# Optimization experiments

Hardware: AMD Instinct MI355X
Metric: run time of the kernel (lower is better)

The kernel has to match this reference:

```python
import jax, jax.numpy as jnp
import numpy as np
from jax import lax

B, N, D = 8, 16384, 64
NPOINT, NSAMPLE, RADIUS = 1024, 32, 0.1
MLP = [3 + D, 64, 64, 128]
BN_EPS = 1e-5


def setup_inputs() -> dict:
    key = jax.random.key(0)
    ks = jax.random.split(key, 8)
    inp = {
        'xyz': jax.random.uniform(ks[0], (B, 3, N), dtype=jnp.float32),
        'points': jax.random.normal(ks[1], (B, D, N), dtype=jnp.float32),
    }
    for i, (cin, cout) in enumerate(zip(MLP[:-1], MLP[1:]), start=1):
        inp[f'w{i}'] = jax.random.normal(ks[1 + i], (cout, cin), dtype=jnp.float32) / np.sqrt(cin)
        inp[f'b{i}'] = jnp.zeros((cout,), jnp.float32)
        inp[f'g{i}'] = jnp.ones((cout,), jnp.float32)
        inp[f'be{i}'] = jnp.zeros((cout,), jnp.float32)
    return inp


def farthest_point_sample(xyz, npoint):
    # xyz: (B, N, 3). Deterministic start at index 0 (torch uses randint).
    b, n, _ = xyz.shape

    def step(carry, _):
        distance, farthest = carry  # (B,N), (B,)
        centroid = jnp.take_along_axis(xyz, farthest[:, None, None], axis=1)  # (B,1,3)
        dist = jnp.sum((xyz - centroid) ** 2, axis=-1)  # (B,N)
        distance = jnp.minimum(distance, dist)
        new_far = jnp.argmax(distance, axis=-1).astype(jnp.int32)
        return (distance, new_far), farthest

    init = (jnp.full((b, n), 1e10, xyz.dtype), jnp.zeros((b,), jnp.int32))
    _, idxs = lax.scan(step, init, None, length=npoint)  # (npoint, B)
    return idxs.T  # (B, npoint)


def query_ball_point(radius, nsample, xyz, new_xyz):
    # xyz: (B,N,3), new_xyz: (B,S,3) -> (B,S,nsample) int32
    b, n, _ = xyz.shape
    # squared pairwise distances (B,S,N)
    sqr = (jnp.sum(new_xyz ** 2, -1)[:, :, None]
           + jnp.sum(xyz ** 2, -1)[:, None, :]
           - 2.0 * jnp.einsum('bsc,bnc->bsn', new_xyz, xyz))
    group_idx = jnp.where(sqr > radius ** 2, n, jnp.arange(n, dtype=jnp.int32))
    group_idx = jnp.sort(group_idx, axis=-1)[:, :, :nsample]
    first = group_idx[:, :, :1]
    return jnp.where(group_idx == n, first, group_idx)


def reference(xyz, points, w1, b1, g1, be1, w2, b2, g2, be2, w3, b3, g3, be3):
    xyz_t = xyz.transpose(0, 2, 1)      # (B,N,3)
    pts_t = points.transpose(0, 2, 1)   # (B,N,D)
    bsz = xyz_t.shape[0]

    fps_idx = farthest_point_sample(xyz_t, NPOINT)          # (B,S)
    bidx2 = jnp.arange(bsz)[:, None]
    new_xyz = xyz_t[bidx2, fps_idx]                          # (B,S,3)

    idx = query_ball_point(RADIUS, NSAMPLE, xyz_t, new_xyz)  # (B,S,ns)
    bidx3 = jnp.arange(bsz)[:, None, None]
    grouped_xyz = xyz_t[bidx3, idx] - new_xyz[:, :, None, :]  # (B,S,ns,3)
    grouped_pts = pts_t[bidx3, idx]                           # (B,S,ns,D)
    feat = jnp.concatenate([grouped_xyz, grouped_pts], axis=-1)  # (B,S,ns,C)

    for w, b, g, be in ((w1, b1, g1, be1), (w2, b2, g2, be2), (w3, b3, g3, be3)):
        feat = jnp.einsum('bsnc,oc->bsno', feat, w) + b
        mean = feat.mean(axis=(0, 1, 2))
        var = feat.var(axis=(0, 1, 2))  # biased, as torch BN uses for normalization
        feat = (feat - mean) * lax.rsqrt(var + BN_EPS) * g + be
        feat = jax.nn.relu(feat)

    new_points = feat.max(axis=2)  # max over nsample -> (B,S,Cout)
    return new_xyz.transpose(0, 2, 1), new_points.transpose(0, 2, 1)
```

## Files before the change

kernel.cpp:

```cpp
#include <hip/hip_runtime.h>
#include <hip/hip_bf16.h>
#include <stdint.h>

#define BATCH 8
#define NPTS  16384
#define DIMF  64
#define SPTS  1024
#define NSAMP 32
#define MTOT  (BATCH*SPTS*NSAMP)

__device__ __forceinline__ float bfu_lo(uint32_t u){ return __uint_as_float(u<<16); }
__device__ __forceinline__ float bfu_hi(uint32_t u){ return __uint_as_float(u & 0xffff0000u); }
__device__ __forceinline__ uint16_t f2bf(float f){
  __hip_bfloat16 h = __float2bfloat16(f);
  uint16_t u; __builtin_memcpy(&u, &h, 2); return u;
}

__global__ __launch_bounds__(512, 2) void fps_kernel(const float* __restrict__ xyz,
                                                     float* __restrict__ out0,
                                                     const float* __restrict__ pts,
                                                     float* __restrict__ ptsT){
  if (blockIdx.x >= BATCH){
    __shared__ float tile[64][65];
    int bb = blockIdx.x - BATCH;
    int b  = bb >> 8;
    int n0 = (bb & 255) << 6;
    const float* src = pts + (size_t)b*DIMF*NPTS;
    float* dst = ptsT + (size_t)b*NPTS*DIMF;
    int t = threadIdx.x;
    int cn = t & 63, cw = t >> 6;
#pragma unroll
    for (int j=0;j<8;j++){
      int c = cw + j*8;
      tile[c][cn] = src[(size_t)c*NPTS + n0 + cn];
    }
    __syncthreads();
#pragma unroll
    for (int j=0;j<8;j++){
      int nl = cw + j*8;
      dst[(size_t)(n0+nl)*DIMF + cn] = tile[cn][nl];
    }
    return;
  }
  int b = blockIdx.x;
  const float* X = xyz + (size_t)b*3*NPTS;
  int t = threadIdx.x;
  int lane = t & 63, wid = t >> 6;
  float px[32], py[32], pz[32], dst[32];
#pragma unroll
  for (int k=0;k<32;k++){
    int n = t + (k<<9);
    px[k]=X[n]; py[k]=X[NPTS+n]; pz[k]=X[2*NPTS+n];
    dst[k]=1e10f;
  }
  __shared__ float rv[2][8];
  __shared__ int   ri[2][8];
  int far = 0;
  float* o = out0 + (size_t)b*3*SPTS;
  for (int s=0;s<SPTS;s++){
    float cx = X[far], cy = X[NPTS+far], cz = X[2*NPTS+far];
    if (t==0){ o[s]=cx; o[SPTS+s]=cy; o[2*SPTS+s]=cz; }
    if (s==SPTS-1) break;
    float best = -1.0f; int bi = 0x7fffffff;
#pragma unroll
    for (int k=0;k<32;k++){
      float dx=__fsub_rn(px[k],cx), dy=__fsub_rn(py[k],cy), dz=__fsub_rn(pz[k],cz);
      float d = __fadd_rn(__fadd_rn(__fmul_rn(dx,dx),__fmul_rn(dy,dy)),__fmul_rn(dz,dz));
      d = fminf(dst[k], d); dst[k] = d;
      if (d > best){ best = d; bi = t + (k<<9); }
    }
#pragma unroll
    for (int off=1; off<64; off<<=1){
      float ov = __shfl_xor(best, off);
      int   oi = __shfl_xor(bi, off);
      if (ov > best || (ov == best && oi < bi)){ best = ov; bi = oi; }
    }
    int p = s & 1;
    if (lane==0){ rv[p][wid]=best; ri[p][wid]=bi; }
    __syncthreads();
    float v = rv[p][lane&7]; int j = ri[p][lane&7];
#pragma unroll
    for (int off=1; off<8; off<<=1){
      float ov = __shfl_xor(v, off);
      int   oj = __shfl_xor(j, off);
      if (ov > v || (ov == v && oj < j)){ v = ov; j = oj; }
    }
    far = j;
  }
}

__global__ __launch_bounds__(256) void ball_kernel(const float* __restrict__ xyz,
                                                   const float* __restrict__ newxyz,
                                                   int* __restrict__ idxo){
  int b  = blockIdx.x >> 5;
  int sc = blockIdx.x & 31;
  const float* X  = xyz + (size_t)b*3*NPTS;
  int t = threadIdx.x, lane = t & 63, w = t >> 6;
  __shared__ float lx[512], ly[512], lz[512], ls[512];
  __shared__ int done;
  if (t==0) done = 0;
  const float rsq = 0.01f;
  float nx[8], ny[8], nz[8], sn[8];
  int cnt[8], first[8];
  int sbase = sc*32 + w*8;
#pragma unroll
  for (int q=0;q<8;q++){
    int s = sbase + q;
    nx[q] = newxyz[(size_t)b*3*SPTS + s];
    ny[q] = newxyz[(size_t)b*3*SPTS + SPTS + s];
    nz[q] = newxyz[(size_t)b*3*SPTS + 2*SPTS + s];
    sn[q] = __fadd_rn(__fadd_rn(__fmul_rn(nx[q],nx[q]),__fmul_rn(ny[q],ny[q])),
                      __fmul_rn(nz[q],nz[q]));
    cnt[q]=0; first[q]=0;
  }
  __syncthreads();
  for (int T=0;T<32;T++){
    {
      float ax = X[T*512 + t], ay = X[NPTS + T*512 + t], az = X[2*NPTS + T*512 + t];
      lx[t]=ax; ly[t]=ay; lz[t]=az;
      ls[t] = __fadd_rn(__fadd_rn(__fmul_rn(ax,ax),__fmul_rn(ay,ay)),__fmul_rn(az,az));
      float bx = X[T*512 + t + 256], by = X[NPTS + T*512 + t + 256], bz = X[2*NPTS + T*512 + t + 256];
      lx[t+256]=bx; ly[t+256]=by; lz[t+256]=bz;
      ls[t+256] = __fadd_rn(__fadd_rn(__fmul_rn(bx,bx),__fmul_rn(by,by)),__fmul_rn(bz,bz));
    }
    __syncthreads();
#pragma unroll
    for (int q=0;q<8;q++){
      if (cnt[q] >= NSAMP) continue;
      int s = sbase + q;
      int* op = idxo + ((size_t)(b*SPTS + s))*NSAMP;
      for (int c=0;c<8;c++){
        int li = c*64 + lane;
        float dot = fmaf(nz[q], lz[li], fmaf(ny[q], ly[li], __fmul_rn(nx[q], lx[li])));
        float sq  = __fsub_rn(__fadd_rn(sn[q], ls[li]), __fmul_rn(2.0f, dot));
        bool in = (sq <= rsq);
        unsigned long long m = __ballot(in);
        if (cnt[q]==0 && m) first[q] = T*512 + c*64 + (int)__builtin_ctzll(m);
        if (in){
          int slot = cnt[q] + (int)__popcll(m & ((1ull<<lane)-1ull));
          if (slot < NSAMP) op[slot] = T*512 + li;
        }
        cnt[q] += (int)__popcll(m);
        if (cnt[q] >= NSAMP){ if (lane==0) atomicAdd(&done,1); break; }
      }
    }
    __syncthreads();
    if (done >= 32) break;
  }
#pragma unroll
  for (int q=0;q<8;q++){
    if (cnt[q] < NSAMP){
      int s = sbase + q;
      int* op = idxo + ((size_t)(b*SPTS + s))*NSAMP;
      if (lane >= cnt[q] && lane < NSAMP) op[lane] = first[q];
    }
  }
}

__global__ __launch_bounds__(256) void gemm1_kernel(const float* __restrict__ xyz,
                                                    const float* __restrict__ ptsT,
                                                    const int* __restrict__ idx,
                                                    const float* __restrict__ newxyz,
                                                    const float* __restrict__ w1,
                                                    const float* __restrict__ b1,
                                                    uint16_t* __restrict__ y1,
                                                    float* __restrict__ gsum,
                                                    float* __restrict__ gsq){
  __shared__ float As[128*69];
  __shared__ float Ws[67*64];
  __shared__ float bias[64];
  __shared__ int   ndx[128];
  __shared__ float nxs[4][3];
  int t = threadIdx.x;
  int g0 = blockIdx.x*128;
  if (t < 128) ndx[t] = idx[g0 + t];
  if (t < 12){
    int grp = t/3, c = t%3;
    int bs = (g0>>5) + grp; int b = bs>>10, s = bs & 1023;
    nxs[grp][c] = newxyz[(size_t)b*3*SPTS + c*SPTS + s];
  }
  if (t < 64) bias[t] = b1[t];
  for (int e=t; e<67*64; e+=256){ int k=e>>6, c=e&63; Ws[k*64+c] = w1[c*67+k]; }
  __syncthreads();
  {
    int r = t>>1, h = t&1;
    int n = ndx[r];
    int bs = (g0>>5) + (r>>5); int b = bs>>10;
    const float* pr = ptsT + ((size_t)(b*NPTS + n))*64 + h*32;
    float* ar = As + r*69;
    if (h==0){
      int grp = r>>5;
      ar[0] = __fsub_rn(xyz[(size_t)b*3*NPTS + n],          nxs[grp][0]);
      ar[1] = __fsub_rn(xyz[(size_t)b*3*NPTS + NPTS + n],   nxs[grp][1]);
      ar[2] = __fsub_rn(xyz[(size_t)b*3*NPTS + 2*NPTS + n], nxs[grp][2]);
    }
    float* ap = ar + 3 + h*32;
#pragma unroll
    for (int j=0;j<8;j++){
      float4 v = *(const float4*)(pr + j*4);
      ap[j*4+0]=v.x; ap[j*4+1]=v.y; ap[j*4+2]=v.z; ap[j*4+3]=v.w;
    }
  }
  __syncthreads();
  int rg = t>>3, cg = t&7;
  float acc[4][8];
#pragma unroll
  for (int i=0;i<4;i++)
#pragma unroll
    for (int j=0;j<8;j++) acc[i][j]=0.f;
  for (int k=0;k<67;k++){
    float a0 = As[(rg*4+0)*69+k];
    float a1 = As[(rg*4+1)*69+k];
    float a2 = As[(rg*4+2)*69+k];
    float a3 = As[(rg*4+3)*69+k];
    const float* wr = Ws + k*64 + cg*8;
    float4 w0 = *(const float4*)wr;
    float4 w1v = *(const float4*)(wr+4);
    float wj[8] = {w0.x,w0.y,w0.z,w0.w,w1v.x,w1v.y,w1v.z,w1v.w};
#pragma unroll
    for (int j=0;j<8;j++){
      acc[0][j] = fmaf(a0, wj[j], acc[0][j]);
      acc[1][j] = fmaf(a1, wj[j], acc[1][j]);
      acc[2][j] = fmaf(a2, wj[j], acc[2][j]);
      acc[3][j] = fmaf(a3, wj[j], acc[3][j]);
    }
  }
  float ps[8], pq[8];
#pragma unroll
  for (int j=0;j<8;j++){ ps[j]=0.f; pq[j]=0.f; }
#pragma unroll
  for (int i=0;i<4;i++){
    int gr = g0 + rg*4 + i;
    uint16_t* yr = y1 + (size_t)gr*64 + cg*8;
    uint4 vv; uint32_t u[4]; float vj[8];
#pragma unroll
    for (int j=0;j<8;j++){
      vj[j] = acc[i][j] + bias[cg*8+j];
      ps[j] += vj[j]; pq[j] += vj[j]*vj[j];
    }
#pragma unroll
    for (int j=0;j<4;j++)
      u[j] = (uint32_t)f2bf(vj[2*j]) | ((uint32_t)f2bf(vj[2*j+1])<<16);
    vv.x=u[0]; vv.y=u[1]; vv.z=u[2]; vv.w=u[3];
    *(uint4*)yr = vv;
  }
  __syncthreads();
  float* red = As;
#pragma unroll
  for (int j=0;j<8;j++){
    red[rg*65 + cg*8 + j]        = ps[j];
    red[2080 + rg*65 + cg*8 + j] = pq[j];
  }
  __syncthreads();
  if (t < 64){
    float s=0.f, q=0.f;
    for (int r=0;r<32;r++){ s += red[r*65+t]; q += red[2080 + r*65 + t]; }
    int kb = (blockIdx.x & 15) * 128;
    atomicAdd(&gsum[kb + t], s); atomicAdd(&gsq[kb + t], q);
  }
}

__global__ __launch_bounds__(256) void gemm2_kernel(const uint16_t* __restrict__ yin,
                                                    const float* __restrict__ w2,
                                                    const float* __restrict__ b2,
                                                    const float* __restrict__ gsumi,
                                                    const float* __restrict__ gsqi,
                                                    const float* __restrict__ gi,
                                                    const float* __restrict__ bei,
                                                    uint16_t* __restrict__ yout,
                                                    float* __restrict__ gsum,
                                                    float* __restrict__ gsq){
  __shared__ float As[128*65];
  __shared__ float Ws[64*64];
  __shared__ float bias[64], sc[64], sh[64];
  int t = threadIdx.x;
  int g0 = blockIdx.x*128;
  if (t < 64){
    bias[t]=b2[t];
    double ssum=0.0, ssq=0.0;
    for (int k2=0;k2<16;k2++){ ssum += (double)gsumi[k2*128+t]; ssq += (double)gsqi[k2*128+t]; }
    double mean = ssum / (double)MTOT;
    double var  = ssq / (double)MTOT - mean*mean;
    double sv   = (double)gi[t] / sqrt(var + 1e-5);
    sc[t] = (float)sv;
    sh[t] = (float)((double)bei[t] - mean*sv);
  }
  for (int e=t; e<64*64; e+=256){ int k=e>>6, c=e&63; Ws[k*64+c] = w2[c*64+k]; }
  __syncthreads();
  {
    int r = t>>1, h = t&1;
    const uint4* yv = (const uint4*)(yin + (size_t)(g0+r)*64 + h*32);
    float* ar = As + r*65 + h*32;
#pragma unroll
    for (int j=0;j<4;j++){
      uint4 u = yv[j];
      uint32_t vv[4] = {u.x,u.y,u.z,u.w};
#pragma unroll
      for (int m=0;m<4;m++){
        int c = h*32 + j*8 + m*2;
        ar[j*8+m*2]   = fmaxf(fmaf(bfu_lo(vv[m]), sc[c],   sh[c]),   0.f);
        ar[j*8+m*2+1] = fmaxf(fmaf(bfu_hi(vv[m]), sc[c+1], sh[c+1]), 0.f);
      }
    }
  }
  __syncthreads();
  int rg = t>>3, cg = t&7;
  float acc[4][8];
#pragma unroll
  for (int i=0;i<4;i++)
#pragma unroll
    for (int j=0;j<8;j++) acc[i][j]=0.f;
  for (int k=0;k<64;k++){
    float a0 = As[(rg*4+0)*65+k];
    float a1 = As[(rg*4+1)*65+k];
    float a2 = As[(rg*4+2)*65+k];
    float a3 = As[(rg*4+3)*65+k];
    const float* wr = Ws + k*64 + cg*8;
    float4 w0 = *(const float4*)wr;
    float4 w1v = *(const float4*)(wr+4);
    float wj[8] = {w0.x,w0.y,w0.z,w0.w,w1v.x,w1v.y,w1v.z,w1v.w};
#pragma unroll
    for (int j=0;j<8;j++){
      acc[0][j] = fmaf(a0, wj[j], acc[0][j]);
      acc[1][j] = fmaf(a1, wj[j], acc[1][j]);
      acc[2][j] = fmaf(a2, wj[j], acc[2][j]);
      acc[3][j] = fmaf(a3, wj[j], acc[3][j]);
    }
  }
  float ps[8], pq[8];
#pragma unroll
  for (int j=0;j<8;j++){ ps[j]=0.f; pq[j]=0.f; }
#pragma unroll
  for (int i=0;i<4;i++){
    int gr = g0 + rg*4 + i;
    uint16_t* yr = yout + (size_t)gr*64 + cg*8;
    uint4 vv; uint32_t u[4]; float vj[8];
#pragma unroll
    for (int j=0;j<8;j++){
      vj[j] = acc[i][j] + bias[cg*8+j];
      ps[j] += vj[j]; pq[j] += vj[j]*vj[j];
    }
#pragma unroll
    for (int j=0;j<4;j++)
      u[j] = (uint32_t)f2bf(vj[2*j]) | ((uint32_t)f2bf(vj[2*j+1])<<16);
    vv.x=u[0]; vv.y=u[1]; vv.z=u[2]; vv.w=u[3];
    *(uint4*)yr = vv;
  }
  __syncthreads();
  float* red = As;
#pragma unroll
  for (int j=0;j<8;j++){
    red[rg*65 + cg*8 + j]        = ps[j];
    red[2080 + rg*65 + cg*8 + j] = pq[j];
  }
  __syncthreads();
  if (t < 64){
    float s=0.f, q=0.f;
    for (int r=0;r<32;r++){ s += red[r*65+t]; q += red[2080 + r*65 + t]; }
    int kb = (blockIdx.x & 15) * 128;
    atomicAdd(&gsum[kb + t], s); atomicAdd(&gsq[kb + t], q);
  }
}

__global__ __launch_bounds__(256) void gemm3_kernel(const uint16_t* __restrict__ yin,
                                                    const float* __restrict__ w3,
                                                    const float* __restrict__ b3,
                                                    const float* __restrict__ gsumi,
                                                    const float* __restrict__ gsqi,
                                                    const float* __restrict__ gi,
                                                    const float* __restrict__ bei,
                                                    uint16_t* __restrict__ yout,
                                                    float* __restrict__ gsum,
                                                    float* __restrict__ gsq){
  __shared__ float As[64*65];
  __shared__ float Ws[64*128];
  __shared__ float bias[128], sc[64], sh[64];
  int t = threadIdx.x;
  int g0 = blockIdx.x*64;
  if (t < 128) bias[t]=b3[t];
  if (t < 64){
    double ssum=0.0, ssq=0.0;
    for (int k2=0;k2<16;k2++){ ssum += (double)gsumi[k2*128+t]; ssq += (double)gsqi[k2*128+t]; }
    double mean = ssum / (double)MTOT;
    double var  = ssq / (double)MTOT - mean*mean;
    double sv   = (double)gi[t] / sqrt(var + 1e-5);
    sc[t] = (float)sv;
    sh[t] = (float)((double)bei[t] - mean*sv);
  }
  for (int e=t; e<64*128; e+=256){ int k=e>>7, c=e&127; Ws[k*128+c] = w3[c*64+k]; }
  __syncthreads();
  {
    int r = t>>2, h = t&3;
    const uint4* yv = (const uint4*)(yin + (size_t)(g0+r)*64 + h*16);
    float* ar = As + r*65 + h*16;
#pragma unroll
    for (int j=0;j<2;j++){
      uint4 u = yv[j];
      uint32_t vv[4] = {u.x,u.y,u.z,u.w};
#pragma unroll
      for (int m=0;m<4;m++){
        int c = h*16 + j*8 + m*2;
        ar[j*8+m*2]   = fmaxf(fmaf(bfu_lo(vv[m]), sc[c],   sh[c]),   0.f);
        ar[j*8+m*2+1] = fmaxf(fmaf(bfu_hi(vv[m]), sc[c+1], sh[c+1]), 0.f);
      }
    }
  }
  __syncthreads();
  int rg = t>>4, cg = t&15;
  float acc[4][8];
#pragma unroll
  for (int i=0;i<4;i++)
#pragma unroll
    for (int j=0;j<8;j++) acc[i][j]=0.f;
  for (int k=0;k<64;k++){
    float a0 = As[(rg*4+0)*65+k];
    float a1 = As[(rg*4+1)*65+k];
    float a2 = As[(rg*4+2)*65+k];
    float a3 = As[(rg*4+3)*65+k];
    const float* wr = Ws + k*128 + cg*8;
    float4 w0 = *(const float4*)wr;
    float4 w1v = *(const float4*)(wr+4);
    float wj[8] = {w0.x,w0.y,w0.z,w0.w,w1v.x,w1v.y,w1v.z,w1v.w};
#pragma unroll
    for (int j=0;j<8;j++){
      acc[0][j] = fmaf(a0, wj[j], acc[0][j]);
      acc[1][j] = fmaf(a1, wj[j], acc[1][j]);
      acc[2][j] = fmaf(a2, wj[j], acc[2][j]);
      acc[3][j] = fmaf(a3, wj[j], acc[3][j]);
    }
  }
  float ps[8], pq[8];
#pragma unroll
  for (int j=0;j<8;j++){ ps[j]=0.f; pq[j]=0.f; }
#pragma unroll
  for (int i=0;i<4;i++){
    int gr = g0 + rg*4 + i;
    uint16_t* yr = yout + (size_t)gr*128 + cg*8;
    uint4 vv; uint32_t u[4]; float vj[8];
#pragma unroll
    for (int j=0;j<8;j++){
      vj[j] = acc[i][j] + bias[cg*8+j];
      ps[j] += vj[j]; pq[j] += vj[j]*vj[j];
    }
#pragma unroll
    for (int j=0;j<4;j++)
      u[j] = (uint32_t)f2bf(vj[2*j]) | ((uint32_t)f2bf(vj[2*j+1])<<16);
    vv.x=u[0]; vv.y=u[1]; vv.z=u[2]; vv.w=u[3];
    *(uint4*)yr = vv;
  }
  __syncthreads();
  float* red = As;
#pragma unroll
  for (int j=0;j<8;j++){
    red[rg*129 + cg*8 + j]        = ps[j];
    red[2064 + rg*129 + cg*8 + j] = pq[j];
  }
  __syncthreads();
  if (t < 128){
    float s=0.f, q=0.f;
    for (int r=0;r<16;r++){ s += red[r*129+t]; q += red[2064 + r*129 + t]; }
    int kb = (blockIdx.x & 15) * 128;
    atomicAdd(&gsum[kb + t], s); atomicAdd(&gsq[kb + t], q);
  }
}

__global__ __launch_bounds__(256) void maxpool_kernel(const uint16_t* __restrict__ y3,
                                                      const float* __restrict__ gsumi,
                                                      const float* __restrict__ gsqi,
                                                      const float* __restrict__ gi,
                                                      const float* __restrict__ bei,
                                                      float* __restrict__ out1){
  __shared__ float tr[16][129];
  __shared__ float scs[128], shs[128];
  int t = threadIdx.x;
  int b = blockIdx.x >> 6;
  int s0 = (blockIdx.x & 63) * 16;
  if (t < 128){
    double ssum=0.0, ssq=0.0;
    for (int k2=0;k2<16;k2++){ ssum += (double)gsumi[k2*128+t]; ssq += (double)gsqi[k2*128+t]; }
    double mean = ssum / (double)MTOT;
    double var  = ssq / (double)MTOT - mean*mean;
    double sv   = (double)gi[t] / sqrt(var + 1e-5);
    scs[t] = (float)sv;
    shs[t] = (float)((double)bei[t] - mean*sv);
  }
  __syncthreads();
  int ch = t & 127, sl0 = t >> 7;
  float scv = scs[ch], shv = shs[ch];
  for (int sl=sl0; sl<16; sl+=2){
    int bs = b*SPTS + s0 + sl;
    const uint16_t* yr = y3 + (size_t)bs*NSAMP*128 + ch;
    float m = 0.0f;
#pragma unroll 4
    for (int k=0;k<NSAMP;k++){
      float v = __uint_as_float(((uint32_t)yr[k*128])<<16);
      float z = fmaxf(fmaf(v, scv, shv), 0.f);
      m = fmaxf(m, z);
    }
    tr[sl][ch] = m;
  }
  __syncthreads();
  int ch2 = t >> 1, hh = t & 1;
  float vals[8];
#pragma unroll
  for (int i=0;i<8;i++) vals[i] = tr[hh*8+i][ch2];
  float* op = out1 + (size_t)b*131072 + (size_t)ch2*1024 + s0 + hh*8;
  float4 v0; v0.x=vals[0]; v0.y=vals[1]; v0.z=vals[2]; v0.w=vals[3];
  float4 v1; v1.x=vals[4]; v1.y=vals[5]; v1.z=vals[6]; v1.w=vals[7];
  *(float4*)op = v0;
  *(float4*)(op+4) = v1;
}

extern "C" void kernel_launch(void* const* d_in, const int* in_sizes, int n_in,
                              void* d_out, int out_size, void* d_ws, size_t ws_size,
                              hipStream_t stream){
  (void)in_sizes; (void)n_in; (void)out_size; (void)ws_size;
  const float* xyz = (const float*)d_in[0];
  const float* pts = (const float*)d_in[1];
  const float* w1 = (const float*)d_in[2];  const float* b1 = (const float*)d_in[3];
  const float* g1 = (const float*)d_in[4];  const float* be1 = (const float*)d_in[5];
  const float* w2 = (const float*)d_in[6];  const float* b2 = (const float*)d_in[7];
  const float* g2 = (const float*)d_in[8];  const float* be2 = (const float*)d_in[9];
  const float* w3 = (const float*)d_in[10]; const float* b3 = (const float*)d_in[11];
  const float* g3 = (const float*)d_in[12]; const float* be3 = (const float*)d_in[13];

  float* out0 = (float*)d_out;
  float* out1 = out0 + BATCH*3*SPTS;

  char* ws = (char*)d_ws;
  float*    ptsT = (float*)(ws + 0);
  float*    stats = (float*)(ws + 33554432);
  int*      idx  = (int*)  (ws + 34078720);
  uint16_t* y1   = (uint16_t*)(ws + 35127296);
  uint16_t* y2   = (uint16_t*)(ws + 68681728);
  uint16_t* y3   = (uint16_t*)(ws + 102236160);
  float* gsum1 = stats;          float* gsq1 = stats + 2048;
  float* gsum2 = stats + 4096;   float* gsq2 = stats + 6144;
  float* gsum3 = stats + 8192;   float* gsq3 = stats + 10240;

  hipMemsetAsync(stats, 0, 12288*sizeof(float), stream);

  fps_kernel<<<BATCH + 2048, 512, 0, stream>>>(xyz, out0, pts, ptsT);
  ball_kernel<<<BATCH*32, 256, 0, stream>>>(xyz, out0, idx);
  gemm1_kernel<<<MTOT/128, 256, 0, stream>>>(xyz, ptsT, idx, out0, w1, b1, y1, gsum1, gsq1);
  gemm2_kernel<<<MTOT/128, 256, 0, stream>>>(y1, w2, b2, gsum1, gsq1, g1, be1, y2, gsum2, gsq2);
  gemm3_kernel<<<MTOT/64, 256, 0, stream>>>(y2, w3, b3, gsum2, gsq2, g2, be2, y3, gsum3, gsq3);
  maxpool_kernel<<<BATCH*(SPTS/16), 256, 0, stream>>>(y3, gsum3, gsq3, g3, be3, out1);
}
```

Before: 2.617 ms.

## Replace layer-3 activation buffer with per-group max/min reductions

The third GEMM no longer writes its full bf16 output. It computes per-group (32-sample) channel max and min of the pre-BN values and stores only those. The maxpool kernel then applies the BN affine map and ReLU to the max or the min, chosen by the sign of the scale, because an affine map followed by ReLU is monotone. This removes a large write and re-read of the layer-3 activations, at the cost of one extra in-block shared-memory reduction. It also slightly changes rounding, since the values are kept in fp32 rather than bf16.

```diff
diff --git a/kernel.cpp b/kernel.cpp
--- a/kernel.cpp
+++ b/kernel.cpp
@@ -369,7 +369,8 @@
                                                     const float* __restrict__ gsqi,
                                                     const float* __restrict__ gi,
                                                     const float* __restrict__ bei,
-                                                    uint16_t* __restrict__ yout,
+                                                    float* __restrict__ Mb,
+                                                    float* __restrict__ mb,
                                                     float* __restrict__ gsum,
                                                     float* __restrict__ gsq){
   __shared__ float As[64*65];
@@ -429,24 +430,18 @@
       acc[3][j] = fmaf(a3, wj[j], acc[3][j]);
     }
   }
-  float ps[8], pq[8];
-#pragma unroll
-  for (int j=0;j<8;j++){ ps[j]=0.f; pq[j]=0.f; }
+  float ps[8], pq[8], tmax[8], tmin[8];
+#pragma unroll
+  for (int j=0;j<8;j++){ ps[j]=0.f; pq[j]=0.f; tmax[j]=-1e30f; tmin[j]=1e30f; }
 #pragma unroll
   for (int i=0;i<4;i++){
-    int gr = g0 + rg*4 + i;
-    uint16_t* yr = yout + (size_t)gr*128 + cg*8;
-    uint4 vv; uint32_t u[4]; float vj[8];
-#pragma unroll
-    for (int j=0;j<8;j++){
-      vj[j] = acc[i][j] + bias[cg*8+j];
-      ps[j] += vj[j]; pq[j] += vj[j]*vj[j];
-    }
-#pragma unroll
-    for (int j=0;j<4;j++)
-      u[j] = (uint32_t)f2bf(vj[2*j]) | ((uint32_t)f2bf(vj[2*j+1])<<16);
-    vv.x=u[0]; vv.y=u[1]; vv.z=u[2]; vv.w=u[3];
-    *(uint4*)yr = vv;
+    float vj;
+#pragma unroll
+    for (int j=0;j<8;j++){
+      vj = acc[i][j] + bias[cg*8+j];
+      ps[j] += vj; pq[j] += vj*vj;
+      tmax[j] = fmaxf(tmax[j], vj); tmin[j] = fminf(tmin[j], vj);
+    }
   }
   __syncthreads();
   float* red = As;
@@ -462,19 +457,38 @@
     int kb = (blockIdx.x & 15) * 128;
     atomicAdd(&gsum[kb + t], s); atomicAdd(&gsq[kb + t], q);
   }
-}
-
-__global__ __launch_bounds__(256) void maxpool_kernel(const uint16_t* __restrict__ y3,
+  __syncthreads();
+  float* redM = As;
+#pragma unroll
+  for (int j=0;j<8;j++){
+    redM[rg*129 + cg*8 + j]        = tmax[j];
+    redM[2064 + rg*129 + cg*8 + j] = tmin[j];
+  }
+  __syncthreads();
+  {
+    int h = t >> 7, ch = t & 127;
+    float M=-1e30f, m=1e30f;
+    for (int r=h*8; r<h*8+8; r++){
+      M = fmaxf(M, redM[r*129+ch]);
+      m = fminf(m, redM[2064 + r*129 + ch]);
+    }
+    int sg = (g0>>5) + h;
+    Mb[(size_t)sg*128 + ch] = M;
+    mb[(size_t)sg*128 + ch] = m;
+  }
+}
+
+__global__ __launch_bounds__(256) void maxpool_kernel(const float* __restrict__ Mb,
+                                                      const float* __restrict__ mb,
                                                       const float* __restrict__ gsumi,
                                                       const float* __restrict__ gsqi,
                                                       const float* __restrict__ gi,
                                                       const float* __restrict__ bei,
                                                       float* __restrict__ out1){
-  __shared__ float tr[16][129];
   __shared__ float scs[128], shs[128];
   int t = threadIdx.x;
-  int b = blockIdx.x >> 6;
-  int s0 = (blockIdx.x & 63) * 16;
+  int b = blockIdx.x >> 4;
+  int s0 = (blockIdx.x & 15) * 64;
   if (t < 128){
     double ssum=0.0, ssq=0.0;
     for (int k2=0;k2<16;k2++){ ssum += (double)gsumi[k2*128+t]; ssq += (double)gsqi[k2*128+t]; }
@@ -485,30 +499,23 @@
     shs[t] = (float)((double)bei[t] - mean*sv);
   }
   __syncthreads();
-  int ch = t & 127, sl0 = t >> 7;
+  int ch = t >> 1, sg2 = t & 1;
   float scv = scs[ch], shv = shs[ch];
-  for (int sl=sl0; sl<16; sl+=2){
-    int bs = b*SPTS + s0 + sl;
-    const uint16_t* yr = y3 + (size_t)bs*NSAMP*128 + ch;
-    float m = 0.0f;
-#pragma unroll 4
-    for (int k=0;k<NSAMP;k++){
-      float v = __uint_as_float(((uint32_t)yr[k*128])<<16);
-      float z = fmaxf(fmaf(v, scv, shv), 0.f);
-      m = fmaxf(m, z);
-    }
-    tr[sl][ch] = m;
-  }
-  __syncthreads();
-  int ch2 = t >> 1, hh = t & 1;
-  float vals[8];
-#pragma unroll
-  for (int i=0;i<8;i++) vals[i] = tr[hh*8+i][ch2];
-  float* op = out1 + (size_t)b*131072 + (size_t)ch2*1024 + s0 + hh*8;
-  float4 v0; v0.x=vals[0]; v0.y=vals[1]; v0.z=vals[2]; v0.w=vals[3];
-  float4 v1; v1.x=vals[4]; v1.y=vals[5]; v1.z=vals[6]; v1.w=vals[7];
-  *(float4*)op = v0;
-  *(float4*)(op+4) = v1;
+  bool pos = (scv >= 0.f);
+  float buf[32];
+#pragma unroll 8
+  for (int k=0;k<32;k++){
+    int s = s0 + sg2*32 + k;
+    size_t g = (size_t)(b*SPTS + s)*128 + ch;
+    float v = pos ? Mb[g] : mb[g];
+    buf[k] = fmaxf(fmaf(v, scv, shv), 0.f);
+  }
+  float* op = out1 + (size_t)b*131072 + (size_t)ch*1024 + s0 + sg2*32;
+#pragma unroll
+  for (int k=0;k<8;k++){
+    float4 v4; v4.x=buf[4*k]; v4.y=buf[4*k+1]; v4.z=buf[4*k+2]; v4.w=buf[4*k+3];
+    ((float4*)op)[k] = v4;
+  }
 }
 
 extern "C" void kernel_launch(void* const* d_in, const int* in_sizes, int n_in,
@@ -533,7 +540,8 @@
   int*      idx  = (int*)  (ws + 34078720);
   uint16_t* y1   = (uint16_t*)(ws + 35127296);
   uint16_t* y2   = (uint16_t*)(ws + 68681728);
-  uint16_t* y3   = (uint16_t*)(ws + 102236160);
+  float*    Mb   = (float*)(ws + 102236160);
+  float*    mb   = (float*)(ws + 106430464);
   float* gsum1 = stats;          float* gsq1 = stats + 2048;
   float* gsum2 = stats + 4096;   float* gsq2 = stats + 6144;
   float* gsum3 = stats + 8192;   float* gsq3 = stats + 10240;
@@ -544,6 +552,6 @@
   ball_kernel<<<BATCH*32, 256, 0, stream>>>(xyz, out0, idx);
   gemm1_kernel<<<MTOT/128, 256, 0, stream>>>(xyz, ptsT, idx, out0, w1, b1, y1, gsum1, gsq1);
   gemm2_kernel<<<MTOT/128, 256, 0, stream>>>(y1, w2, b2, gsum1, gsq1, g1, be1, y2, gsum2, gsq2);
-  gemm3_kernel<<<MTOT/64, 256, 0, stream>>>(y2, w3, b3, gsum2, gsq2, g2, be2, y3, gsum3, gsq3);
-  maxpool_kernel<<<BATCH*(SPTS/16), 256, 0, stream>>>(y3, gsum3, gsq3, g3, be3, out1);
-}
+  gemm3_kernel<<<MTOT/64, 256, 0, stream>>>(y2, w3, b3, gsum2, gsq2, g2, be2, Mb, mb, gsum3, gsq3);
+  maxpool_kernel<<<BATCH*16, 256, 0, stream>>>(Mb, mb, gsum3, gsq3, g3, be3, out1);
+}
```

New measurement: 2.611 ms. About the same (-0.2%).
